# Optimization experiments

Hardware: AMD Instinct MI355X
Metric: run time of the kernel (lower is better)

The kernel has to match this reference:

```python
import jax, jax.numpy as jnp
import numpy as np

NNODES = 8192
DIM = 64
K = 32
ALPHA = 3.0


def setup_inputs() -> dict:
    key = jax.random.key(0)
    ks = jax.random.split(key, 7)
    idx = jnp.arange(NNODES, dtype=jnp.int64)
    # xavier_uniform for 2D params, uniform[0,1) for biases (per _reset_parameters)
    def xavier(k, shape):
        fan_in, fan_out = shape[1], shape[0]
        bound = float(np.sqrt(6.0 / (fan_in + fan_out)))
        return jax.random.uniform(k, shape, jnp.float32, -bound, bound)
    E1 = xavier(ks[0], (NNODES, DIM))
    E2 = xavier(ks[1], (NNODES, DIM))
    W1 = xavier(ks[2], (DIM, DIM))
    b1 = jax.random.uniform(ks[3], (DIM,), jnp.float32)
    W2 = xavier(ks[4], (DIM, DIM))
    b2 = jax.random.uniform(ks[5], (DIM,), jnp.float32)
    return {"idx": idx, "E1": E1, "E2": E2, "W1": W1, "b1": b1, "W2": W2, "b2": b2}


def reference(idx, E1, E2, W1, b1, W2, b2):
    n = idx.shape[0]
    # embedding lookups [n, dim]
    v1 = E1[idx]
    v2 = E2[idx]
    # linear (torch: x @ W.T + b) then tanh saturation
    v1 = jnp.tanh(ALPHA * (v1 @ W1.T + b1))
    v2 = jnp.tanh(ALPHA * (v2 @ W2.T + b2))
    # antisymmetric score matrix [n, n]
    a = v1 @ v2.T - v2 @ v1.T
    A = jax.nn.relu(jnp.tanh(ALPHA * a))
    # top-k per row -> binary mask via scatter
    _, t1 = jax.lax.top_k(A, K)  # [n, K]
    rows = jnp.arange(n)[:, None]
    mask = jnp.zeros((n, n), A.dtype).at[rows, t1].set(1.0)
    return A * mask
```

## Files before the change

### kernel.cpp

```cpp
#include <hip/hip_runtime.h>
#include <stdint.h>
#include <math.h>

#define NN 8192
#define DIM 64
#define KSEL 32
#define BK2 16
#define TILE 128
#define NTB (NN / TILE)
#define NTRI ((NTB * (NTB + 1)) / 2)

__device__ __forceinline__ float tanh_xla(float x) {
    const float kClamp = 7.90531110763549805f;
    float xc = fminf(fmaxf(x, -kClamp), kClamp);
    float x2 = xc * xc;
    float p = -2.76076847742355e-16f;
    p = fmaf(x2, p, 2.00018790482477e-13f);
    p = fmaf(x2, p, -8.60467152213735e-11f);
    p = fmaf(x2, p, 5.12229709037114e-08f);
    p = fmaf(x2, p, 1.48572235717979e-05f);
    p = fmaf(x2, p, 6.37261928875436e-04f);
    p = fmaf(x2, p, 4.89352455891786e-03f);
    p = xc * p;
    float q = 1.19825839466702e-06f;
    q = fmaf(x2, q, 1.18534705686654e-04f);
    q = fmaf(x2, q, 2.26843463243900e-03f);
    q = fmaf(x2, q, 4.89352518554385e-03f);
    float r = p / q;
    return (fabsf(x) < 0.0004f) ? x : r;
}
__device__ __forceinline__ float tanh_xla_pos(float ax) {
    const float kClamp = 7.90531110763549805f;
    float xc = fminf(ax, kClamp);
    float x2 = xc * xc;
    float p = -2.76076847742355e-16f;
    p = fmaf(x2, p, 2.00018790482477e-13f);
    p = fmaf(x2, p, -8.60467152213735e-11f);
    p = fmaf(x2, p, 5.12229709037114e-08f);
    p = fmaf(x2, p, 1.48572235717979e-05f);
    p = fmaf(x2, p, 6.37261928875436e-04f);
    p = fmaf(x2, p, 4.89352455891786e-03f);
    p = xc * p;
    float q = 1.19825839466702e-06f;
    q = fmaf(x2, q, 1.18534705686654e-04f);
    q = fmaf(x2, q, 2.26843463243900e-03f);
    q = fmaf(x2, q, 4.89352518554385e-03f);
    float r = p / q;
    return (ax < 0.0004f) ? ax : r;
}

__global__ __launch_bounds__(256) void k_embed(
    const int* __restrict__ gidx,
    const float* __restrict__ E1, const float* __restrict__ E2,
    const float* __restrict__ W1, const float* __restrict__ b1,
    const float* __restrict__ W2, const float* __restrict__ b2,
    float* __restrict__ V1, float* __restrict__ V2)
{
    __shared__ float W1s[DIM][DIM + 1];
    __shared__ float W2s[DIM][DIM + 1];
    __shared__ float E1s[4][DIM];
    __shared__ float E2s[4][DIM];
    const int t = threadIdx.x;
    for (int i = t; i < DIM * DIM; i += 256) {
        W1s[i >> 6][i & 63] = W1[i];
        W2s[i >> 6][i & 63] = W2[i];
    }
    const int rbase = blockIdx.x * 4;
    for (int i = t; i < 4 * DIM; i += 256) {
        const int r = i >> 6, k = i & 63;
        const int g = gidx[rbase + r];
        E1s[r][k] = E1[(size_t)g * DIM + k];
        E2s[r][k] = E2[(size_t)g * DIM + k];
    }
    __syncthreads();
    const int o = t & 63, rs = t >> 6;
    float m1 = 0.0f, m2 = 0.0f;
    #pragma unroll
    for (int k = 0; k < DIM; ++k) {
        m1 = fmaf(E1s[rs][k], W1s[o][k], m1);
        m2 = fmaf(E2s[rs][k], W2s[o][k], m2);
    }
    V1[(size_t)(rbase + rs) * DIM + o] = tanh_xla(3.0f * (m1 + b1[o]));
    V2[(size_t)(rbase + rs) * DIM + o] = tanh_xla(3.0f * (m2 + b2[o]));
}

__global__ __launch_bounds__(256) void k_score(
    const float* __restrict__ V1, const float* __restrict__ V2,
    float* __restrict__ out)
{
    const int L = blockIdx.x;
    int bi = (int)(64.5f - sqrtf(fmaf(-2.0f, (float)L, 64.5f * 64.5f)));
    while (bi * NTB - (bi * (bi - 1)) / 2 > L) --bi;
    while ((bi + 1) * NTB - ((bi + 1) * bi) / 2 <= L) ++bi;
    const int bj = bi + (L - (bi * NTB - (bi * (bi - 1)) / 2));

    __shared__ float sA1[BK2][TILE];
    __shared__ float sA2[BK2][TILE];
    __shared__ float sB1[BK2][TILE];
    __shared__ float sB2[BK2][TILE];

    const int t = threadIdx.x;
    const int tx = t & 15;
    const int ty = t >> 4;
    const int Ibase = bi * TILE, Jbase = bj * TILE;

    float acc1[8][8], acc2[8][8];
    #pragma unroll
    for (int i = 0; i < 8; ++i)
        #pragma unroll
        for (int j = 0; j < 8; ++j) { acc1[i][j] = 0.0f; acc2[i][j] = 0.0f; }

    for (int ck = 0; ck < DIM; ck += BK2) {
        __syncthreads();
        #pragma unroll
        for (int it = 0; it < 2; ++it) {
            const int idx = it * 256 + t;
            const int r   = idx & 127;
            const int c4  = idx >> 7;
            float4 f;
            f = *(const float4*)&V1[(size_t)(Ibase + r) * DIM + ck + c4 * 4];
            sA1[c4*4+0][r]=f.x; sA1[c4*4+1][r]=f.y; sA1[c4*4+2][r]=f.z; sA1[c4*4+3][r]=f.w;
            f = *(const float4*)&V2[(size_t)(Ibase + r) * DIM + ck + c4 * 4];
            sA2[c4*4+0][r]=f.x; sA2[c4*4+1][r]=f.y; sA2[c4*4+2][r]=f.z; sA2[c4*4+3][r]=f.w;
            f = *(const float4*)&V1[(size_t)(Jbase + r) * DIM + ck + c4 * 4];
            sB1[c4*4+0][r]=f.x; sB1[c4*4+1][r]=f.y; sB1[c4*4+2][r]=f.z; sB1[c4*4+3][r]=f.w;
            f = *(const float4*)&V2[(size_t)(Jbase + r) * DIM + ck + c4 * 4];
            sB2[c4*4+0][r]=f.x; sB2[c4*4+1][r]=f.y; sB2[c4*4+2][r]=f.z; sB2[c4*4+3][r]=f.w;
        }
        __syncthreads();
        #pragma unroll 2
        for (int k = 0; k < BK2; ++k) {
            float a1[8], a2[8], c1[8], c2[8];
            *(float4*)&a1[0] = *(const float4*)&sA1[k][ty * 8];
            *(float4*)&a1[4] = *(const float4*)&sA1[k][ty * 8 + 4];
            *(float4*)&a2[0] = *(const float4*)&sA2[k][ty * 8];
            *(float4*)&a2[4] = *(const float4*)&sA2[k][ty * 8 + 4];
            *(float4*)&c1[0] = *(const float4*)&sB1[k][tx * 4];
            *(float4*)&c1[4] = *(const float4*)&sB1[k][tx * 4 + 64];
            *(float4*)&c2[0] = *(const float4*)&sB2[k][tx * 4];
            *(float4*)&c2[4] = *(const float4*)&sB2[k][tx * 4 + 64];
            #pragma unroll
            for (int i = 0; i < 8; ++i)
                #pragma unroll
                for (int j = 0; j < 8; ++j) {
                    acc1[i][j] = fmaf(a1[i], c2[j], acc1[i][j]);
                    acc2[i][j] = fmaf(a2[i], c1[j], acc2[i][j]);
                }
        }
    }
    #pragma unroll
    for (int i = 0; i < 8; ++i)
        #pragma unroll
        for (int j = 0; j < 8; ++j) {
            const float aa = acc1[i][j] - acc2[i][j];
            const float tt = tanh_xla_pos(3.0f * fabsf(aa));
            acc1[i][j] = (aa > 0.0f) ? tt : 0.0f;
            acc2[i][j] = (aa < 0.0f) ? tt : 0.0f;
        }
    #pragma unroll
    for (int i = 0; i < 8; ++i) {
        const int gi = Ibase + ty * 8 + i;
        *(float4*)&out[(size_t)gi * NN + Jbase + tx * 4] =
            make_float4(acc1[i][0], acc1[i][1], acc1[i][2], acc1[i][3]);
        *(float4*)&out[(size_t)gi * NN + Jbase + 64 + tx * 4] =
            make_float4(acc1[i][4], acc1[i][5], acc1[i][6], acc1[i][7]);
    }
    if (bi != bj) {
        #pragma unroll
        for (int j = 0; j < 8; ++j) {
            const int gj = Jbase + tx * 4 + (j >> 2) * 64 + (j & 3);
            float4* p = (float4*)&out[(size_t)gj * NN + Ibase + ty * 8];
            p[0] = make_float4(acc2[0][j], acc2[1][j], acc2[2][j], acc2[3][j]);
            p[1] = make_float4(acc2[4][j], acc2[5][j], acc2[6][j], acc2[7][j]);
        }
    }
}

__global__ __launch_bounds__(256) void k_topk(float* __restrict__ out)
{
    __shared__ uint32_t hist[4][2048];
    __shared__ uint32_t waveTot[4];
    __shared__ uint32_t bc_bin, bc_ca, bc_m, bc_flag;

    const int row = blockIdx.x;
    const int t = threadIdx.x;
    const int wid = t >> 6, lane = t & 63;
    float* rp = out + (size_t)row * NN;

    float v[32];
    #pragma unroll
    for (int s = 0; s < 8; ++s) {
        const float4 f = *(const float4*)&rp[(s * 256 + t) * 4];
        v[s*4+0] = f.x; v[s*4+1] = f.y; v[s*4+2] = f.z; v[s*4+3] = f.w;
    }
    if (t == 0) bc_flag = 0;

    uint64_t prefix = 0, thr = 0;
    int need = KSEL;
    bool done = false;

    for (int pass = 0; pass < 4; ++pass) {
        const int shift = 33 - 11 * pass;
        {
            const uint4 z = make_uint4(0u, 0u, 0u, 0u);
            uint4* hp = (uint4*)hist;
            #pragma unroll
            for (int i = 0; i < 8; ++i) hp[i * 256 + t] = z;
        }
        __syncthreads();
        #pragma unroll
        for (int s = 0; s < 8; ++s) {
            #pragma unroll
            for (int e = 0; e < 4; ++e) {
                const uint32_t vb = __float_as_uint(v[s*4+e]);
                if (vb == 0u) continue;
                const int gi = s * 1024 + t * 4 + e;
                const uint64_t key = ((uint64_t)vb << 13) | (uint32_t)(8191 - gi);
                if ((key >> (shift + 11)) == prefix)
                    atomicAdd(&hist[wid][(uint32_t)((key >> shift) & 2047u)], 1u);
            }
        }
        __syncthreads();
        uint32_t m[8]; uint32_t tot = 0;
        #pragma unroll
        for (int i = 0; i < 8; ++i) {
            const int b = t * 8 + i;
            m[i] = hist[0][b] + hist[1][b] + hist[2][b] + hist[3][b];
            tot += m[i];
        }
        uint32_t ssum = tot;
        #pragma unroll
        for (int d = 1; d < 64; d <<= 1) {
            const uint32_t o = __shfl_down(ssum, d, 64);
            if (lane + d < 64) ssum += o;
        }
        if (lane == 0) waveTot[wid] = ssum;
        __syncthreads();
        {
            uint32_t above = 0;
            for (int w2 = wid + 1; w2 < 4; ++w2) above += waveTot[w2];
            if (pass == 0) {
                const uint32_t totalAll = waveTot[0] + waveTot[1] + waveTot[2] + waveTot[3];
                if (totalAll < (uint32_t)need && t == 0) bc_flag = 1;
            }
            uint32_t c = (ssum - tot) + above;
            #pragma unroll
            for (int i = 7; i >= 0; --i) {
                if (c < (uint32_t)need && (uint32_t)need <= c + m[i]) {
                    bc_bin = (uint32_t)(t * 8 + i);
                    bc_ca  = c;
                    bc_m   = m[i];
                }
                c += m[i];
            }
        }
        __syncthreads();
        if (bc_flag) { thr = 1; done = true; }
        else {
            prefix = (prefix << 11) | (uint64_t)bc_bin;
            need  -= (int)bc_ca;
            if ((uint32_t)need == bc_m) {
                thr = prefix << shift;
                done = true;
            } else if (pass == 3) { thr = prefix; done = true; }
        }
        if (done) break;
        __syncthreads();
    }

    #pragma unroll
    for (int s = 0; s < 8; ++s) {
        float w[4];
        #pragma unroll
        for (int e = 0; e < 4; ++e) {
            const float a = v[s*4+e];
            const uint32_t vb = __float_as_uint(a);
            const int gi = s * 1024 + t * 4 + e;
            const uint64_t key = ((uint64_t)vb << 13) | (uint32_t)(8191 - gi);
            w[e] = (vb != 0u && key >= thr) ? a : 0.f;
        }
        *(float4*)&rp[(s * 256 + t) * 4] = make_float4(w[0], w[1], w[2], w[3]);
    }
}

extern "C" void kernel_launch(void* const* d_in, const int* in_sizes, int n_in,
                              void* d_out, int out_size, void* d_ws, size_t ws_size,
                              hipStream_t stream)
{
    const int*   idx = (const int*)  d_in[0];
    const float* E1  = (const float*)d_in[1];
    const float* E2  = (const float*)d_in[2];
    const float* W1  = (const float*)d_in[3];
    const float* b1  = (const float*)d_in[4];
    const float* W2  = (const float*)d_in[5];
    const float* b2  = (const float*)d_in[6];
    float* out = (float*)d_out;
    float* V1 = (float*)d_ws;
    float* V2 = V1 + (size_t)NN * DIM;

    k_embed<<<NN / 4, 256, 0, stream>>>(idx, E1, E2, W1, b1, W2, b2, V1, V2);
    k_score<<<NTRI, 256, 0, stream>>>(V1, V2, out);
    k_topk<<<NN, 256, 0, stream>>>(out);
}
```

Before: 298.8 us.

## Transpose embeddings and double-buffer score tiles via direct global-to-LDS loads with packed FMA

The embedding kernel now writes V1/V2 transposed (dim-major) through a small shared staging tile. The score kernel uses that layout to load tiles straight into double-buffered LDS with global_load_lds, prefetching the next K-chunk while computing the current one. The inner product is also rewritten with 2-wide packed FMAs. The aim is to remove the register transpose on load, overlap memory with compute, and halve the FMA instruction count. The cost is extra LDS, and the transposed embedding stores are strided.

Result: faster. 281.4 us (-5.8%).

```diff
diff --git a/kernel.cpp b/kernel.cpp
--- a/kernel.cpp
+++ b/kernel.cpp
@@ -9,6 +9,18 @@
 #define TILE 128
 #define NTB (NN / TILE)
 #define NTRI ((NTB * (NTB + 1)) / 2)
+
+#define AS1 __attribute__((address_space(1)))
+#define AS3 __attribute__((address_space(3)))
+typedef float v2f __attribute__((ext_vector_type(2)));
+
+__device__ __forceinline__ v2f pk_fma(v2f a, v2f b, v2f c) {
+#if __has_builtin(__builtin_elementwise_fma)
+    return __builtin_elementwise_fma(a, b, c);
+#else
+    v2f r; r.x = fmaf(a.x, b.x, c.x); r.y = fmaf(a.y, b.y, c.y); return r;
+#endif
+}
 
 __device__ __forceinline__ float tanh_xla(float x) {
     const float kClamp = 7.90531110763549805f;
@@ -54,12 +66,14 @@
     const float* __restrict__ E1, const float* __restrict__ E2,
     const float* __restrict__ W1, const float* __restrict__ b1,
     const float* __restrict__ W2, const float* __restrict__ b2,
-    float* __restrict__ V1, float* __restrict__ V2)
+    float* __restrict__ VT1, float* __restrict__ VT2)
 {
     __shared__ float W1s[DIM][DIM + 1];
     __shared__ float W2s[DIM][DIM + 1];
     __shared__ float E1s[4][DIM];
     __shared__ float E2s[4][DIM];
+    __shared__ float T1[DIM][5];
+    __shared__ float T2[DIM][5];
     const int t = threadIdx.x;
     for (int i = t; i < DIM * DIM; i += 256) {
         W1s[i >> 6][i & 63] = W1[i];
@@ -80,12 +94,16 @@
         m1 = fmaf(E1s[rs][k], W1s[o][k], m1);
         m2 = fmaf(E2s[rs][k], W2s[o][k], m2);
     }
-    V1[(size_t)(rbase + rs) * DIM + o] = tanh_xla(3.0f * (m1 + b1[o]));
-    V2[(size_t)(rbase + rs) * DIM + o] = tanh_xla(3.0f * (m2 + b2[o]));
+    T1[o][rs] = tanh_xla(3.0f * (m1 + b1[o]));
+    T2[o][rs] = tanh_xla(3.0f * (m2 + b2[o]));
+    __syncthreads();
+    const int oo = t >> 2, rr = t & 3;
+    VT1[(size_t)oo * NN + rbase + rr] = T1[oo][rr];
+    VT2[(size_t)oo * NN + rbase + rr] = T2[oo][rr];
 }
 
 __global__ __launch_bounds__(256) void k_score(
-    const float* __restrict__ V1, const float* __restrict__ V2,
+    const float* __restrict__ VT1, const float* __restrict__ VT2,
     float* __restrict__ out)
 {
     const int L = blockIdx.x;
@@ -94,84 +112,103 @@
     while ((bi + 1) * NTB - ((bi + 1) * bi) / 2 <= L) ++bi;
     const int bj = bi + (L - (bi * NTB - (bi * (bi - 1)) / 2));
 
-    __shared__ float sA1[BK2][TILE];
-    __shared__ float sA2[BK2][TILE];
-    __shared__ float sB1[BK2][TILE];
-    __shared__ float sB2[BK2][TILE];
+    __shared__ __align__(16) float lds[2][4][BK2][TILE];
 
     const int t = threadIdx.x;
     const int tx = t & 15;
     const int ty = t >> 4;
     const int Ibase = bi * TILE, Jbase = bj * TILE;
 
-    float acc1[8][8], acc2[8][8];
+    const int w = t >> 6, l = t & 63;
+    const float* vt = (w & 1) ? VT2 : VT1;
+    const int cbase = (w & 2) ? Jbase : Ibase;
+    const int srow = (l >> 5);
+    const int scol = (l & 31) * 4;
+
+    v2f acc1[8][4], acc2[8][4];
     #pragma unroll
     for (int i = 0; i < 8; ++i)
         #pragma unroll
-        for (int j = 0; j < 8; ++j) { acc1[i][j] = 0.0f; acc2[i][j] = 0.0f; }
-
-    for (int ck = 0; ck < DIM; ck += BK2) {
-        __syncthreads();
-        #pragma unroll
-        for (int it = 0; it < 2; ++it) {
-            const int idx = it * 256 + t;
-            const int r   = idx & 127;
-            const int c4  = idx >> 7;
-            float4 f;
-            f = *(const float4*)&V1[(size_t)(Ibase + r) * DIM + ck + c4 * 4];
-            sA1[c4*4+0][r]=f.x; sA1[c4*4+1][r]=f.y; sA1[c4*4+2][r]=f.z; sA1[c4*4+3][r]=f.w;
-            f = *(const float4*)&V2[(size_t)(Ibase + r) * DIM + ck + c4 * 4];
-            sA2[c4*4+0][r]=f.x; sA2[c4*4+1][r]=f.y; sA2[c4*4+2][r]=f.z; sA2[c4*4+3][r]=f.w;
-            f = *(const float4*)&V1[(size_t)(Jbase + r) * DIM + ck + c4 * 4];
-            sB1[c4*4+0][r]=f.x; sB1[c4*4+1][r]=f.y; sB1[c4*4+2][r]=f.z; sB1[c4*4+3][r]=f.w;
-            f = *(const float4*)&V2[(size_t)(Jbase + r) * DIM + ck + c4 * 4];
-            sB2[c4*4+0][r]=f.x; sB2[c4*4+1][r]=f.y; sB2[c4*4+2][r]=f.z; sB2[c4*4+3][r]=f.w;
-        }
-        __syncthreads();
+        for (int j = 0; j < 4; ++j) { acc1[i][j] = (v2f)(0.0f); acc2[i][j] = (v2f)(0.0f); }
+
+    #pragma unroll
+    for (int p = 0; p < 8; ++p) {
+        const float* src = vt + (size_t)(2 * p + srow) * NN + cbase + scol;
+        __builtin_amdgcn_global_load_lds((AS1 const void*)src,
+                                         (AS3 void*)&lds[0][w][2 * p + srow][scol], 16, 0, 0);
+    }
+    __syncthreads();
+
+    for (int c4 = 0; c4 < 4; ++c4) {
+        const int cur = c4 & 1;
+        if (c4 < 3) {
+            const int ckn = (c4 + 1) * BK2;
+            #pragma unroll
+            for (int p = 0; p < 8; ++p) {
+                const float* src = vt + (size_t)(ckn + 2 * p + srow) * NN + cbase + scol;
+                __builtin_amdgcn_global_load_lds((AS1 const void*)src,
+                                                 (AS3 void*)&lds[cur ^ 1][w][2 * p + srow][scol], 16, 0, 0);
+            }
+        }
         #pragma unroll 2
         for (int k = 0; k < BK2; ++k) {
-            float a1[8], a2[8], c1[8], c2[8];
-            *(float4*)&a1[0] = *(const float4*)&sA1[k][ty * 8];
-            *(float4*)&a1[4] = *(const float4*)&sA1[k][ty * 8 + 4];
-            *(float4*)&a2[0] = *(const float4*)&sA2[k][ty * 8];
-            *(float4*)&a2[4] = *(const float4*)&sA2[k][ty * 8 + 4];
-            *(float4*)&c1[0] = *(const float4*)&sB1[k][tx * 4];
-            *(float4*)&c1[4] = *(const float4*)&sB1[k][tx * 4 + 64];
-            *(float4*)&c2[0] = *(const float4*)&sB2[k][tx * 4];
-            *(float4*)&c2[4] = *(const float4*)&sB2[k][tx * 4 + 64];
-            #pragma unroll
-            for (int i = 0; i < 8; ++i)
+            const float4 fa1l = *(const float4*)&lds[cur][0][k][ty * 8];
+            const float4 fa1h = *(const float4*)&lds[cur][0][k][ty * 8 + 4];
+            const float4 fa2l = *(const float4*)&lds[cur][1][k][ty * 8];
+            const float4 fa2h = *(const float4*)&lds[cur][1][k][ty * 8 + 4];
+            const float4 fb1l = *(const float4*)&lds[cur][2][k][tx * 4];
+            const float4 fb1h = *(const float4*)&lds[cur][2][k][tx * 4 + 64];
+            const float4 fb2l = *(const float4*)&lds[cur][3][k][tx * 4];
+            const float4 fb2h = *(const float4*)&lds[cur][3][k][tx * 4 + 64];
+            v2f c1p[4], c2p[4];
+            c1p[0] = (v2f){fb1l.x, fb1l.y}; c1p[1] = (v2f){fb1l.z, fb1l.w};
+            c1p[2] = (v2f){fb1h.x, fb1h.y}; c1p[3] = (v2f){fb1h.z, fb1h.w};
+            c2p[0] = (v2f){fb2l.x, fb2l.y}; c2p[1] = (v2f){fb2l.z, fb2l.w};
+            c2p[2] = (v2f){fb2h.x, fb2h.y}; c2p[3] = (v2f){fb2h.z, fb2h.w};
+            float a1[8] = {fa1l.x, fa1l.y, fa1l.z, fa1l.w, fa1h.x, fa1h.y, fa1h.z, fa1h.w};
+            float a2[8] = {fa2l.x, fa2l.y, fa2l.z, fa2l.w, fa2h.x, fa2h.y, fa2h.z, fa2h.w};
+            #pragma unroll
+            for (int i = 0; i < 8; ++i) {
+                const v2f a1v = (v2f){a1[i], a1[i]};
+                const v2f a2v = (v2f){a2[i], a2[i]};
                 #pragma unroll
-                for (int j = 0; j < 8; ++j) {
-                    acc1[i][j] = fmaf(a1[i], c2[j], acc1[i][j]);
-                    acc2[i][j] = fmaf(a2[i], c1[j], acc2[i][j]);
+                for (int jp = 0; jp < 4; ++jp) {
+                    acc1[i][jp] = pk_fma(a1v, c2p[jp], acc1[i][jp]);
+                    acc2[i][jp] = pk_fma(a2v, c1p[jp], acc2[i][jp]);
                 }
-        }
-    }
+            }
+        }
+        __syncthreads();
+    }
+
+    float wn[8][8], wm[8][8];
     #pragma unroll
     for (int i = 0; i < 8; ++i)
         #pragma unroll
-        for (int j = 0; j < 8; ++j) {
-            const float aa = acc1[i][j] - acc2[i][j];
-            const float tt = tanh_xla_pos(3.0f * fabsf(aa));
-            acc1[i][j] = (aa > 0.0f) ? tt : 0.0f;
-            acc2[i][j] = (aa < 0.0f) ? tt : 0.0f;
-        }
+        for (int jp = 0; jp < 4; ++jp)
+            #pragma unroll
+            for (int e = 0; e < 2; ++e) {
+                const int j = jp * 2 + e;
+                const float aa = acc1[i][jp][e] - acc2[i][jp][e];
+                const float tt = tanh_xla_pos(3.0f * fabsf(aa));
+                wn[i][j] = (aa > 0.0f) ? tt : 0.0f;
+                wm[i][j] = (aa < 0.0f) ? tt : 0.0f;
+            }
     #pragma unroll
     for (int i = 0; i < 8; ++i) {
         const int gi = Ibase + ty * 8 + i;
         *(float4*)&out[(size_t)gi * NN + Jbase + tx * 4] =
-            make_float4(acc1[i][0], acc1[i][1], acc1[i][2], acc1[i][3]);
+            make_float4(wn[i][0], wn[i][1], wn[i][2], wn[i][3]);
         *(float4*)&out[(size_t)gi * NN + Jbase + 64 + tx * 4] =
-            make_float4(acc1[i][4], acc1[i][5], acc1[i][6], acc1[i][7]);
+            make_float4(wn[i][4], wn[i][5], wn[i][6], wn[i][7]);
     }
     if (bi != bj) {
         #pragma unroll
         for (int j = 0; j < 8; ++j) {
             const int gj = Jbase + tx * 4 + (j >> 2) * 64 + (j & 3);
             float4* p = (float4*)&out[(size_t)gj * NN + Ibase + ty * 8];
-            p[0] = make_float4(acc2[0][j], acc2[1][j], acc2[2][j], acc2[3][j]);
-            p[1] = make_float4(acc2[4][j], acc2[5][j], acc2[6][j], acc2[7][j]);
+            p[0] = make_float4(wm[0][j], wm[1][j], wm[2][j], wm[3][j]);
+            p[1] = make_float4(wm[4][j], wm[5][j], wm[6][j], wm[7][j]);
         }
     }
 }
@@ -295,10 +332,10 @@
     const float* W2  = (const float*)d_in[5];
     const float* b2  = (const float*)d_in[6];
     float* out = (float*)d_out;
-    float* V1 = (float*)d_ws;
-    float* V2 = V1 + (size_t)NN * DIM;
-
-    k_embed<<<NN / 4, 256, 0, stream>>>(idx, E1, E2, W1, b1, W2, b2, V1, V2);
-    k_score<<<NTRI, 256, 0, stream>>>(V1, V2, out);
+    float* VT1 = (float*)d_ws;
+    float* VT2 = VT1 + (size_t)NN * DIM;
+
+    k_embed<<<NN / 4, 256, 0, stream>>>(idx, E1, E2, W1, b1, W2, b2, VT1, VT2);
+    k_score<<<NTRI, 256, 0, stream>>>(VT1, VT2, out);
     k_topk<<<NN, 256, 0, stream>>>(out);
 }
```
